# Optimization experiments

Measured on AMD Instinct MI355X. Metric: run time of the kernel, lower is better.

Reference implementation:

```python
import jax, jax.numpy as jnp
import numpy as np

SENT_LEN = 512
CTX_LEN = 256
NUM_SEGMENTS = 2048  # fixed output rows (torch version uses 1+segment_ids.max(); fixed here for jit)


def setup_inputs() -> dict:
    key = jax.random.key(0)
    kx, ks = jax.random.split(key)
    x = jax.random.normal(kx, (32, 1024, 1024), dtype=jnp.float32)
    # segment ids in [-1, NUM_SEGMENTS-1]; -1 marks invalid (masked) tokens
    segment_ids = jax.random.randint(ks, (32, 1024), -1, NUM_SEGMENTS, dtype=jnp.int64)
    return {"x": x, "segment_ids": segment_ids}


def reference(x, segment_ids):
    lo, hi = 1 + CTX_LEN, 1 + SENT_LEN + CTX_LEN
    emb = x[:, lo:hi, :]                                   # [B, S, D]
    cls = jnp.broadcast_to(x[:, 0:1, :], emb.shape)        # with_cls_embeddings
    emb = jnp.concatenate([emb, cls], axis=-1)             # [B, S, 2D]
    seg = segment_ids[:, lo:hi]                            # [B, S]

    segf = seg.reshape(-1)                                 # [B*S]
    embf = emb.reshape(-1, emb.shape[-1])                  # [B*S, 2D]
    valid = segf >= 0
    # route invalid rows to an overflow bucket that we slice off
    seg_safe = jnp.where(valid, segf, NUM_SEGMENTS)
    w = valid.astype(embf.dtype)
    sums = jax.ops.segment_sum(embf * w[:, None], seg_safe,
                               num_segments=NUM_SEGMENTS + 1)[:NUM_SEGMENTS]
    counts = jax.ops.segment_sum(w, seg_safe,
                                 num_segments=NUM_SEGMENTS + 1)[:NUM_SEGMENTS]
    # scatter_mean: segments with zero count yield 0 (matches torch_scatter)
    return sums / jnp.maximum(counts, 1.0)[:, None]       # [NUM_SEGMENTS, 2D]
```

## Files before the change

### kernel.cpp

```cpp
#include <hip/hip_runtime.h>

#define NBATCH 32
#define NSEG 2048
#define LO 257
#define XROW 1024
#define XBATCH (1024 * 1024)
#define SEGROW 1024
#define MAXTOK 64

__global__ __launch_bounds__(256) void k_fused(const float* __restrict__ x,
                                               const int* __restrict__ seg_ids,
                                               float* __restrict__ out) {
    __shared__ int toks[MAXTOK];
    __shared__ int s_cntb[NBATCH];
    __shared__ int s_cnt;
    const int seg = blockIdx.x;
    const int tid = threadIdx.x;
    if (tid < NBATCH) s_cntb[tid] = 0;
    if (tid == 0) s_cnt = 0;
    __syncthreads();

    const int4* seg4 = (const int4*)seg_ids;
#pragma unroll 4
    for (int v = tid; v < NBATCH * 128; v += 256) {
        int b = v >> 7, j = v & 127;
        int4 q = seg4[b * (SEGROW / 4) + 64 + j];
        int rbase = 256 + 4 * j;
        int ids[4] = {q.x, q.y, q.z, q.w};
#pragma unroll
        for (int k = 0; k < 4; k++) {
            int r = rbase + k;
            if (r >= LO && ids[k] == seg) {
                int p = atomicAdd(&s_cnt, 1);
                if (p < MAXTOK) toks[p] = b * 512 + (r - LO);
                atomicAdd(&s_cntb[b], 1);
            }
        }
    }
    if (tid < NBATCH) {
        int s = seg_ids[tid * SEGROW + 768];
        if (s == seg) {
            int p = atomicAdd(&s_cnt, 1);
            if (p < MAXTOK) toks[p] = tid * 512 + 511;
            atomicAdd(&s_cntb[tid], 1);
        }
    }
    __syncthreads();
    int n = s_cnt;
    int n8 = n > MAXTOK ? MAXTOK : n;

    float4 a1 = make_float4(0.f, 0.f, 0.f, 0.f);
    float4 a2 = make_float4(0.f, 0.f, 0.f, 0.f);
    for (int i = 0; i < n8; i++) {
        int id = toks[i];
        int b = id >> 9, t = id & 511;
        float4 e = ((const float4*)(x + (size_t)b * XBATCH + (size_t)(LO + t) * XROW))[tid];
        a1.x += e.x; a1.y += e.y; a1.z += e.z; a1.w += e.w;
    }
#pragma unroll
    for (int b = 0; b < NBATCH; b++) {
        int c = s_cntb[b];
        if (c > 0) {
            float fc = (float)c;
            float4 cl = ((const float4*)(x + (size_t)b * XBATCH))[tid];
            a2.x += fc * cl.x; a2.y += fc * cl.y; a2.z += fc * cl.z; a2.w += fc * cl.w;
        }
    }
    float inv = (n > 0) ? (1.0f / (float)n) : 1.0f;
    a1.x *= inv; a1.y *= inv; a1.z *= inv; a1.w *= inv;
    a2.x *= inv; a2.y *= inv; a2.z *= inv; a2.w *= inv;

    float4* o = (float4*)(out + (size_t)seg * 2048);
    o[tid] = a1;
    o[256 + tid] = a2;
}

extern "C" void kernel_launch(void* const* d_in, const int* in_sizes, int n_in,
                              void* d_out, int out_size, void* d_ws, size_t ws_size,
                              hipStream_t stream) {
    const float* x = (const float*)d_in[0];
    const int* seg_ids = (const int*)d_in[1];
    float* out = (float*)d_out;
    k_fused<<<NSEG, 256, 0, stream>>>(x, seg_ids, out);
}
```

Baseline: 192.3 us.

## Process four segments per block to share segment-id scan and CLS loads

Each block now handles four consecutive segments instead of one, so the full scan of the segment-id window is done once per four segments and each CLS row load is shared across all four accumulators. Token gathers are unrolled four at a time with nontemporal loads, and output writes use nontemporal stores. The grid shrinks to a quarter of the blocks, which lowers parallelism and increases register use per thread.

Measured after the change: 193.1 us. About the same (+0.4%).

```diff
diff --git a/kernel.cpp b/kernel.cpp
--- a/kernel.cpp
+++ b/kernel.cpp
@@ -7,17 +7,22 @@
 #define XBATCH (1024 * 1024)
 #define SEGROW 1024
 #define MAXTOK 64
+#define GROUP 4
+#define NBLK (NSEG / GROUP)
+
+typedef float f4 __attribute__((ext_vector_type(4)));
 
 __global__ __launch_bounds__(256) void k_fused(const float* __restrict__ x,
                                                const int* __restrict__ seg_ids,
                                                float* __restrict__ out) {
-    __shared__ int toks[MAXTOK];
-    __shared__ int s_cntb[NBATCH];
-    __shared__ int s_cnt;
-    const int seg = blockIdx.x;
+    __shared__ int toks[GROUP][MAXTOK];
+    __shared__ int s_cnt[GROUP];
+    __shared__ int s_cntb[GROUP][NBATCH];
+    const int seg0 = blockIdx.x * GROUP;
     const int tid = threadIdx.x;
-    if (tid < NBATCH) s_cntb[tid] = 0;
-    if (tid == 0) s_cnt = 0;
+
+    if (tid < GROUP * NBATCH) ((int*)s_cntb)[tid] = 0;
+    if (tid < GROUP) s_cnt[tid] = 0;
     __syncthreads();
 
     const int4* seg4 = (const int4*)seg_ids;
@@ -30,49 +35,72 @@
 #pragma unroll
         for (int k = 0; k < 4; k++) {
             int r = rbase + k;
-            if (r >= LO && ids[k] == seg) {
-                int p = atomicAdd(&s_cnt, 1);
-                if (p < MAXTOK) toks[p] = b * 512 + (r - LO);
-                atomicAdd(&s_cntb[b], 1);
+            unsigned g = (unsigned)(ids[k] - seg0);
+            if (g < GROUP && r >= LO) {
+                int p = atomicAdd(&s_cnt[g], 1);
+                if (p < MAXTOK) toks[g][p] = (b << 9) | (r - LO);
+                atomicAdd(&s_cntb[g][b], 1);
             }
         }
     }
     if (tid < NBATCH) {
-        int s = seg_ids[tid * SEGROW + 768];
-        if (s == seg) {
-            int p = atomicAdd(&s_cnt, 1);
-            if (p < MAXTOK) toks[p] = tid * 512 + 511;
-            atomicAdd(&s_cntb[tid], 1);
+        unsigned g = (unsigned)(seg_ids[tid * SEGROW + 768] - seg0);
+        if (g < GROUP) {
+            int p = atomicAdd(&s_cnt[g], 1);
+            if (p < MAXTOK) toks[g][p] = (tid << 9) | 511;
+            atomicAdd(&s_cntb[g][tid], 1);
         }
     }
     __syncthreads();
-    int n = s_cnt;
-    int n8 = n > MAXTOK ? MAXTOK : n;
 
-    float4 a1 = make_float4(0.f, 0.f, 0.f, 0.f);
-    float4 a2 = make_float4(0.f, 0.f, 0.f, 0.f);
-    for (int i = 0; i < n8; i++) {
-        int id = toks[i];
-        int b = id >> 9, t = id & 511;
-        float4 e = ((const float4*)(x + (size_t)b * XBATCH + (size_t)(LO + t) * XROW))[tid];
-        a1.x += e.x; a1.y += e.y; a1.z += e.z; a1.w += e.w;
-    }
+    f4 a1[GROUP], a2[GROUP];
 #pragma unroll
-    for (int b = 0; b < NBATCH; b++) {
-        int c = s_cntb[b];
-        if (c > 0) {
-            float fc = (float)c;
-            float4 cl = ((const float4*)(x + (size_t)b * XBATCH))[tid];
-            a2.x += fc * cl.x; a2.y += fc * cl.y; a2.z += fc * cl.z; a2.w += fc * cl.w;
+    for (int g = 0; g < GROUP; g++) { a1[g] = 0.f; a2[g] = 0.f; }
+
+#pragma unroll
+    for (int g = 0; g < GROUP; g++) {
+        int n = s_cnt[g];
+        int n8 = n > MAXTOK ? MAXTOK : n;
+        int i = 0;
+        for (; i + 4 <= n8; i += 4) {
+            int id0 = toks[g][i + 0], id1 = toks[g][i + 1];
+            int id2 = toks[g][i + 2], id3 = toks[g][i + 3];
+            const f4* p0 = (const f4*)(x + (size_t)(id0 >> 9) * XBATCH + (size_t)(LO + (id0 & 511)) * XROW);
+            const f4* p1 = (const f4*)(x + (size_t)(id1 >> 9) * XBATCH + (size_t)(LO + (id1 & 511)) * XROW);
+            const f4* p2 = (const f4*)(x + (size_t)(id2 >> 9) * XBATCH + (size_t)(LO + (id2 & 511)) * XROW);
+            const f4* p3 = (const f4*)(x + (size_t)(id3 >> 9) * XBATCH + (size_t)(LO + (id3 & 511)) * XROW);
+            f4 e0 = __builtin_nontemporal_load(p0 + tid);
+            f4 e1 = __builtin_nontemporal_load(p1 + tid);
+            f4 e2 = __builtin_nontemporal_load(p2 + tid);
+            f4 e3 = __builtin_nontemporal_load(p3 + tid);
+            a1[g] += (e0 + e1) + (e2 + e3);
+        }
+        for (; i < n8; i++) {
+            int id = toks[g][i];
+            const f4* p = (const f4*)(x + (size_t)(id >> 9) * XBATCH + (size_t)(LO + (id & 511)) * XROW);
+            a1[g] += __builtin_nontemporal_load(p + tid);
         }
     }
-    float inv = (n > 0) ? (1.0f / (float)n) : 1.0f;
-    a1.x *= inv; a1.y *= inv; a1.z *= inv; a1.w *= inv;
-    a2.x *= inv; a2.y *= inv; a2.z *= inv; a2.w *= inv;
 
-    float4* o = (float4*)(out + (size_t)seg * 2048);
-    o[tid] = a1;
-    o[256 + tid] = a2;
+    for (int b = 0; b < NBATCH; b++) {
+        int c0 = s_cntb[0][b], c1 = s_cntb[1][b], c2 = s_cntb[2][b], c3 = s_cntb[3][b];
+        if ((c0 | c1 | c2 | c3) != 0) {
+            f4 cl = ((const f4*)(x + (size_t)b * XBATCH))[tid];
+            a2[0] += (float)c0 * cl;
+            a2[1] += (float)c1 * cl;
+            a2[2] += (float)c2 * cl;
+            a2[3] += (float)c3 * cl;
+        }
+    }
+
+#pragma unroll
+    for (int g = 0; g < GROUP; g++) {
+        int n = s_cnt[g];
+        float inv = (n > 0) ? (1.0f / (float)n) : 1.0f;
+        f4* o = (f4*)(out + (size_t)(seg0 + g) * 2048);
+        __builtin_nontemporal_store(a1[g] * inv, o + tid);
+        __builtin_nontemporal_store(a2[g] * inv, o + 256 + tid);
+    }
 }
 
 extern "C" void kernel_launch(void* const* d_in, const int* in_sizes, int n_in,
@@ -81,5 +109,5 @@
     const float* x = (const float*)d_in[0];
     const int* seg_ids = (const int*)d_in[1];
     float* out = (float*)d_out;
-    k_fused<<<NSEG, 256, 0, stream>>>(x, seg_ids, out);
+    k_fused<<<NBLK, 256, 0, stream>>>(x, seg_ids, out);
 }
```

## Split segment scan into global bucketing pass and per-segment gather kernel

Applied to the files above, without the earlier changes.

Replaces the per-block full rescan of all segment ids (each of 2048 blocks reads the whole 64KB id slice) with a separate scan kernel that buckets token indices per segment via global atomics, followed by a gather kernel that reads only its own bucket. The gather loop is unrolled by four with nontemporal loads and stores so more row loads are in flight. This removes redundant id reads and the per-block scan latency, at the cost of two extra kernel launches and workspace traffic. It falls back to the fused kernel if no workspace is available. Token order within a bucket now depends on atomic order, so the floating-point summation order is nondeterministic.

Measured after the change: 187.1 us. 1.03x faster.

```diff
diff --git a/kernel.cpp b/kernel.cpp
--- a/kernel.cpp
+++ b/kernel.cpp
@@ -7,19 +7,93 @@
 #define XBATCH (1024 * 1024)
 #define SEGROW 1024
 #define MAXTOK 64
+#define NTOKTOT (NBATCH * 512)
+
+typedef float f4 __attribute__((ext_vector_type(4)));
+
+
+__global__ __launch_bounds__(256) void k_zero(int* __restrict__ cnt) {
+    cnt[blockIdx.x * 256 + threadIdx.x] = 0;
+}
+
+__global__ __launch_bounds__(256) void k_scan(const int* __restrict__ seg_ids,
+                                              int* __restrict__ cnt,
+                                              int* __restrict__ toks) {
+    int v = blockIdx.x * 256 + threadIdx.x;
+    int b = v >> 9, t = v & 511;
+    int s = seg_ids[b * SEGROW + LO + t];
+    if (s >= 0) {
+        int p = atomicAdd(&cnt[s], 1);
+        if (p < MAXTOK) toks[s * MAXTOK + p] = v;
+    }
+}
+
+__global__ __launch_bounds__(256) void k_gather(const float* __restrict__ x,
+                                                const int* __restrict__ cnt,
+                                                const int* __restrict__ toks,
+                                                float* __restrict__ out) {
+    __shared__ int s_tok[MAXTOK];
+    __shared__ int s_cntb[NBATCH];
+    const int seg = blockIdx.x;
+    const int tid = threadIdx.x;
+    if (tid < NBATCH) s_cntb[tid] = 0;
+    __syncthreads();
+    int ntrue = cnt[seg];
+    int n = ntrue > MAXTOK ? MAXTOK : ntrue;
+    if (tid < n) {
+        int v = toks[seg * MAXTOK + tid];
+        s_tok[tid] = v;
+        atomicAdd(&s_cntb[v >> 9], 1);
+    }
+    __syncthreads();
+
+    f4 a1 = 0.f, a2 = 0.f;
+    int i = 0;
+    for (; i + 4 <= n; i += 4) {
+        int v0 = s_tok[i + 0], v1 = s_tok[i + 1], v2 = s_tok[i + 2], v3 = s_tok[i + 3];
+        const f4* p0 = (const f4*)(x + (size_t)(v0 >> 9) * XBATCH + (size_t)(LO + (v0 & 511)) * XROW);
+        const f4* p1 = (const f4*)(x + (size_t)(v1 >> 9) * XBATCH + (size_t)(LO + (v1 & 511)) * XROW);
+        const f4* p2 = (const f4*)(x + (size_t)(v2 >> 9) * XBATCH + (size_t)(LO + (v2 & 511)) * XROW);
+        const f4* p3 = (const f4*)(x + (size_t)(v3 >> 9) * XBATCH + (size_t)(LO + (v3 & 511)) * XROW);
+        f4 e0 = __builtin_nontemporal_load(p0 + tid);
+        f4 e1 = __builtin_nontemporal_load(p1 + tid);
+        f4 e2 = __builtin_nontemporal_load(p2 + tid);
+        f4 e3 = __builtin_nontemporal_load(p3 + tid);
+        a1 += (e0 + e1) + (e2 + e3);
+    }
+    for (; i < n; i++) {
+        int v = s_tok[i];
+        const f4* p = (const f4*)(x + (size_t)(v >> 9) * XBATCH + (size_t)(LO + (v & 511)) * XROW);
+        a1 += __builtin_nontemporal_load(p + tid);
+    }
+
+#pragma unroll
+    for (int b = 0; b < NBATCH; b++) {
+        int c = s_cntb[b];
+        if (c > 0) {
+            f4 cl = ((const f4*)(x + (size_t)b * XBATCH))[tid];
+            a2 += (float)c * cl;
+        }
+    }
+
+    float inv = (ntrue > 0) ? (1.0f / (float)ntrue) : 1.0f;
+    f4* o = (f4*)(out + (size_t)seg * 2048);
+    __builtin_nontemporal_store(a1 * inv, o + tid);
+    __builtin_nontemporal_store(a2 * inv, o + 256 + tid);
+}
+
 
 __global__ __launch_bounds__(256) void k_fused(const float* __restrict__ x,
                                                const int* __restrict__ seg_ids,
                                                float* __restrict__ out) {
-    __shared__ int toks[MAXTOK];
-    __shared__ int s_cntb[NBATCH];
-    __shared__ int s_cnt;
+    __shared__ int ftoks[MAXTOK];
+    __shared__ int f_cntb[NBATCH];
+    __shared__ int f_cnt;
     const int seg = blockIdx.x;
     const int tid = threadIdx.x;
-    if (tid < NBATCH) s_cntb[tid] = 0;
-    if (tid == 0) s_cnt = 0;
+    if (tid < NBATCH) f_cntb[tid] = 0;
+    if (tid == 0) f_cnt = 0;
     __syncthreads();
-
     const int4* seg4 = (const int4*)seg_ids;
 #pragma unroll 4
     for (int v = tid; v < NBATCH * 128; v += 256) {
@@ -31,48 +105,41 @@
         for (int k = 0; k < 4; k++) {
             int r = rbase + k;
             if (r >= LO && ids[k] == seg) {
-                int p = atomicAdd(&s_cnt, 1);
-                if (p < MAXTOK) toks[p] = b * 512 + (r - LO);
-                atomicAdd(&s_cntb[b], 1);
+                int p = atomicAdd(&f_cnt, 1);
+                if (p < MAXTOK) ftoks[p] = (b << 9) | (r - LO);
+                atomicAdd(&f_cntb[b], 1);
             }
         }
     }
     if (tid < NBATCH) {
         int s = seg_ids[tid * SEGROW + 768];
         if (s == seg) {
-            int p = atomicAdd(&s_cnt, 1);
-            if (p < MAXTOK) toks[p] = tid * 512 + 511;
-            atomicAdd(&s_cntb[tid], 1);
+            int p = atomicAdd(&f_cnt, 1);
+            if (p < MAXTOK) ftoks[p] = (tid << 9) | 511;
+            atomicAdd(&f_cntb[tid], 1);
         }
     }
     __syncthreads();
-    int n = s_cnt;
+    int n = f_cnt;
     int n8 = n > MAXTOK ? MAXTOK : n;
-
-    float4 a1 = make_float4(0.f, 0.f, 0.f, 0.f);
-    float4 a2 = make_float4(0.f, 0.f, 0.f, 0.f);
+    f4 a1 = 0.f, a2 = 0.f;
     for (int i = 0; i < n8; i++) {
-        int id = toks[i];
-        int b = id >> 9, t = id & 511;
-        float4 e = ((const float4*)(x + (size_t)b * XBATCH + (size_t)(LO + t) * XROW))[tid];
-        a1.x += e.x; a1.y += e.y; a1.z += e.z; a1.w += e.w;
+        int id = ftoks[i];
+        const f4* p = (const f4*)(x + (size_t)(id >> 9) * XBATCH + (size_t)(LO + (id & 511)) * XROW);
+        a1 += p[tid];
     }
 #pragma unroll
     for (int b = 0; b < NBATCH; b++) {
-        int c = s_cntb[b];
+        int c = f_cntb[b];
         if (c > 0) {
-            float fc = (float)c;
-            float4 cl = ((const float4*)(x + (size_t)b * XBATCH))[tid];
-            a2.x += fc * cl.x; a2.y += fc * cl.y; a2.z += fc * cl.z; a2.w += fc * cl.w;
+            f4 cl = ((const f4*)(x + (size_t)b * XBATCH))[tid];
+            a2 += (float)c * cl;
         }
     }
     float inv = (n > 0) ? (1.0f / (float)n) : 1.0f;
-    a1.x *= inv; a1.y *= inv; a1.z *= inv; a1.w *= inv;
-    a2.x *= inv; a2.y *= inv; a2.z *= inv; a2.w *= inv;
-
-    float4* o = (float4*)(out + (size_t)seg * 2048);
-    o[tid] = a1;
-    o[256 + tid] = a2;
+    f4* o = (f4*)(out + (size_t)seg * 2048);
+    o[tid] = a1 * inv;
+    o[256 + tid] = a2 * inv;
 }
 
 extern "C" void kernel_launch(void* const* d_in, const int* in_sizes, int n_in,
@@ -81,5 +148,14 @@
     const float* x = (const float*)d_in[0];
     const int* seg_ids = (const int*)d_in[1];
     float* out = (float*)d_out;
-    k_fused<<<NSEG, 256, 0, stream>>>(x, seg_ids, out);
+    size_t need = (size_t)(NSEG + NSEG * MAXTOK) * sizeof(int);
+    if (d_ws != nullptr && ws_size >= need) {
+        int* cnt = (int*)d_ws;
+        int* toks = cnt + NSEG;
+        k_zero<<<NSEG / 256, 256, 0, stream>>>(cnt);
+        k_scan<<<NTOKTOT / 256, 256, 0, stream>>>(seg_ids, cnt, toks);
+        k_gather<<<NSEG, 256, 0, stream>>>(x, cnt, toks, out);
+    } else {
+        k_fused<<<NSEG, 256, 0, stream>>>(x, seg_ids, out);
+    }
 }
```
